# Kernel tuning notes

Measured on AMD Instinct MI355X. Metric: run time of the kernel, lower is better.

## Reference

```python
import jax, jax.numpy as jnp
import numpy as np

N_NODES = 100_000
N_EDGES = 1_200_000
IN_C, HID_C, OUT_C, K = 64, 64, 32, 3


def setup_inputs() -> dict:
    key = jax.random.key(0)
    ks = jax.random.split(key, 8)
    x = jax.random.normal(ks[0], (N_NODES, IN_C), dtype=jnp.float32)
    edge_index = jax.random.randint(ks[1], (2, N_EDGES), 0, N_NODES, dtype=jnp.int64)
    # ChebConv parameters: weight [K, in, out], bias [out] (Glorot-ish scale)
    W1 = jax.random.normal(ks[2], (K, IN_C, HID_C), dtype=jnp.float32) / np.sqrt(IN_C)
    b1 = jnp.zeros((HID_C,), dtype=jnp.float32)
    W2 = jax.random.normal(ks[3], (K, HID_C, OUT_C), dtype=jnp.float32) / np.sqrt(HID_C)
    b2 = jnp.zeros((OUT_C,), dtype=jnp.float32)
    return {"x": x, "edge_index": edge_index, "W1": W1, "b1": b1, "W2": W2, "b2": b2}


def _cheb_conv(x, row, col, norm_w, W, b):
    # Scaled Laplacian with lambda_max=2 (PyG default): L_hat = -D^{-1/2} A D^{-1/2}
    def prop(t):  # L_hat @ t, via edge gather + segment-sum scatter
        msg = norm_w[:, None] * t[col]            # [E, C]
        return -jax.ops.segment_sum(msg, row, num_segments=N_NODES)

    Tx0 = x
    out = Tx0 @ W[0]
    Tx1 = prop(x)
    out = out + Tx1 @ W[1]
    for k in range(2, W.shape[0]):
        Tx2 = 2.0 * prop(Tx1) - Tx0          # Chebyshev recurrence
        out = out + Tx2 @ W[k]
        Tx0, Tx1 = Tx1, Tx2
    return out + b


def reference(x, edge_index, W1, b1, W2, b2):
    row, col = edge_index[0], edge_index[1]
    deg = jax.ops.segment_sum(jnp.ones((row.shape[0],), x.dtype), row,
                              num_segments=N_NODES)
    deg_inv_sqrt = jnp.where(deg > 0, jax.lax.rsqrt(jnp.maximum(deg, 1.0)), 0.0)
    norm_w = deg_inv_sqrt[row] * deg_inv_sqrt[col]   # symmetric normalization

    h = jax.nn.relu(_cheb_conv(x, row, col, norm_w, W1, b1))
    # dropout omitted (eval mode / training=False)
    return _cheb_conv(h, row, col, norm_w, W2, b2)
```

## Files before the change

kernel.cpp:

```cpp
#include <hip/hip_runtime.h>
#include <hip/hip_fp16.h>

#define N_NODES_C 100000
#define N_EDGES_C 1200000
#define NBUK ((N_NODES_C + 255) >> 8)
#define CHUNK 4096

typedef _Float16 f16x8 __attribute__((ext_vector_type(8)));
typedef float f32x4 __attribute__((ext_vector_type(4)));

#define PACK(r8, c) ((c) | ((r8) << 17))
#define UNPACK_C(v) ((v) & 0x1FFFF)
#define UNPACK_R(v) ((v) >> 17)

__global__ __launch_bounds__(256) void hist_f2h(const int* __restrict__ ei,
                                                int* __restrict__ bucket_cnt,
                                                const float* __restrict__ x,
                                                __half* __restrict__ xh,
                                                int nedges, int n4, int histB) {
    __shared__ int cnt[NBUK];
    const int tid = threadIdx.x;
    if (blockIdx.x < histB) {
        const int base = blockIdx.x * CHUNK;
        const int nloc = min(CHUNK, nedges - base);
        for (int i = tid; i < NBUK; i += 256) cnt[i] = 0;
        __syncthreads();
        for (int i = tid; i < nloc; i += 256) atomicAdd(&cnt[ei[base + i] >> 8], 1);
        __syncthreads();
        for (int b = tid; b < NBUK; b += 256) {
            int n = cnt[b];
            if (n) atomicAdd(&bucket_cnt[b], n);
        }
    } else {
        int i = (blockIdx.x - histB) * 256 + tid;
        if (i < n4) {
            float4 v = ((const float4*)x)[i];
            __half2 tmp[2];
            tmp[0] = __floats2half2_rn(v.x, v.y);
            tmp[1] = __floats2half2_rn(v.z, v.w);
            ((float2*)xh)[i] = *(float2*)tmp;
        }
    }
}

__global__ __launch_bounds__(256) void scan_fold(const int* __restrict__ bucket_cnt,
                                                 int* __restrict__ bucket_base,
                                                 int* __restrict__ bucket_next, int nb,
                                                 const float* __restrict__ W1,
                                                 const float* __restrict__ W2,
                                                 __half* __restrict__ W1f,
                                                 __half* __restrict__ W2f) {
    const int tid = threadIdx.x;
    if (blockIdx.x == 0) {
        __shared__ int s[256];
        int a0 = (2 * tid < nb) ? bucket_cnt[2 * tid] : 0;
        int a1 = (2 * tid + 1 < nb) ? bucket_cnt[2 * tid + 1] : 0;
        s[tid] = a0 + a1;
        __syncthreads();
        for (int off = 1; off < 256; off <<= 1) {
            int v = s[tid];
            int add = (tid >= off) ? s[tid - off] : 0;
            __syncthreads();
            s[tid] = v + add;
            __syncthreads();
        }
        int excl = (tid > 0) ? s[tid - 1] : 0;
        if (2 * tid < nb) { bucket_base[2 * tid] = excl; bucket_next[2 * tid] = excl; }
        if (2 * tid + 1 < nb) { bucket_base[2 * tid + 1] = excl + a0; bucket_next[2 * tid + 1] = excl + a0; }
        if (tid == 255) bucket_base[nb] = s[255];
        return;
    }
    int i = (blockIdx.x - 1) * 256 + tid;
    if (i < 12288) {
        int j = i & 7;
        int lane = (i >> 3) & 63;
        int rest = i >> 9;
        int kh = rest % 6;
        int ct = rest / 6;
        int term = kh >> 1;
        int k = ((kh & 1) << 5) | ((lane >> 4) << 3) | j;
        int c = (ct << 4) | (lane & 15);
        float w0 = W1[k * 64 + c];
        float w1 = W1[4096 + k * 64 + c];
        float w2 = W1[2 * 4096 + k * 64 + c];
        float v = (term == 0) ? (w0 - w2) : ((term == 1) ? w1 : 2.0f * w2);
        W1f[i] = __float2half(v);
    } else if (i < 12288 + 6144) {
        int ii = i - 12288;
        int j = ii & 7;
        int lane = (ii >> 3) & 63;
        int rest = ii >> 9;
        int kh = rest & 1;
        int ct = rest >> 1;
        int k = (kh << 5) | ((lane >> 4) << 3) | j;
        int cg = ct * 16 + (lane & 15);
        int seg = cg >> 5;
        int c = cg & 31;
        float w0 = W2[k * 32 + c];
        float w1 = W2[2048 + k * 32 + c];
        float w2 = W2[2 * 2048 + k * 32 + c];
        float v = (seg == 0) ? (w0 - w2) : ((seg == 1) ? w1 : 2.0f * w2);
        W2f[ii] = __float2half(v);
    }
}

__global__ __launch_bounds__(256) void bin_stage(const int* __restrict__ ei,
                                                 int* __restrict__ bucket_next,
                                                 int* __restrict__ staged, int nedges) {
    __shared__ int cnt[NBUK];
    __shared__ int ofs[NBUK];
    __shared__ int run[NBUK];
    __shared__ int gbase[NBUK];
    __shared__ int ssum[256];
    __shared__ int2 sedge[CHUNK];
    const int tid = threadIdx.x;
    const int base = blockIdx.x * CHUNK;
    const int nloc = min(CHUNK, nedges - base);

    for (int i = tid; i < NBUK; i += 256) { cnt[i] = 0; run[i] = 0; }
    __syncthreads();

    int r[16], c[16];
#pragma unroll
    for (int k = 0; k < 16; ++k) {
        int loc = tid + k * 256;
        bool ok = loc < nloc;
        int idx = base + loc;
        r[k] = ok ? ei[idx] : -1;
        c[k] = ok ? ei[nedges + idx] : 0;
        if (ok) atomicAdd(&cnt[r[k] >> 8], 1);
    }
    __syncthreads();

    int a0 = (2 * tid < NBUK) ? cnt[2 * tid] : 0;
    int a1 = (2 * tid + 1 < NBUK) ? cnt[2 * tid + 1] : 0;
    ssum[tid] = a0 + a1;
    __syncthreads();
    for (int off = 1; off < 256; off <<= 1) {
        int v = ssum[tid];
        int add = (tid >= off) ? ssum[tid - off] : 0;
        __syncthreads();
        ssum[tid] = v + add;
        __syncthreads();
    }
    int excl = (tid > 0) ? ssum[tid - 1] : 0;
    if (2 * tid < NBUK) ofs[2 * tid] = excl;
    if (2 * tid + 1 < NBUK) ofs[2 * tid + 1] = excl + a0;
    __syncthreads();

#pragma unroll
    for (int k = 0; k < 16; ++k) {
        if (r[k] >= 0) {
            int b = r[k] >> 8;
            int p = atomicAdd(&run[b], 1);
            sedge[ofs[b] + p] = make_int2(r[k], c[k]);
        }
    }
    __syncthreads();

    for (int b = tid; b < NBUK; b += 256) {
        int n = cnt[b];
        gbase[b] = n ? atomicAdd(&bucket_next[b], n) : 0;
    }
    __syncthreads();

    for (int i = tid; i < nloc; i += 256) {
        int2 e = sedge[i];
        int b = e.x >> 8;
        staged[gbase[b] + (i - ofs[b])] = PACK(e.x & 255, e.y);
    }
}

__global__ __launch_bounds__(256) void bin_count(const int* __restrict__ staged,
                                                 const int* __restrict__ bucket_base,
                                                 int* __restrict__ rowptr, float* __restrict__ dis,
                                                 int nnodes, int nedges) {
    __shared__ int deg[256];
    __shared__ int ssum[256];
    const int b = blockIdx.x;
    const int n0 = b << 8;
    const int nend = min(n0 + 256, nnodes);
    const int nloc = nend - n0;
    const int tid = threadIdx.x;
    deg[tid] = 0;
    __syncthreads();
    const int ebase = bucket_base[b];
    const int ecount = bucket_base[b + 1] - ebase;
    for (int i = tid; i < ecount; i += 256) {
        atomicAdd(&deg[UNPACK_R(staged[ebase + i])], 1);
    }
    __syncthreads();
    int d = deg[tid];
    if (tid < nloc) {
        float df = (float)d;
        dis[n0 + tid] = (d > 0) ? (1.0f / sqrtf(fmaxf(df, 1.f))) : 0.f;
    }
    ssum[tid] = d;
    __syncthreads();
    for (int off = 1; off < 256; off <<= 1) {
        int v = ssum[tid];
        int add = (tid >= off) ? ssum[tid - off] : 0;
        __syncthreads();
        ssum[tid] = v + add;
        __syncthreads();
    }
    int excl = (tid > 0) ? ssum[tid - 1] : 0;
    if (tid < nloc) rowptr[n0 + tid] = ebase + excl;
    if (b == NBUK - 1 && tid == 0) rowptr[nnodes] = nedges;
}

__global__ __launch_bounds__(256) void bin_place(const int* __restrict__ staged,
                                                 const int* __restrict__ rowptr,
                                                 const float* __restrict__ dis,
                                                 int2* __restrict__ colw, int nnodes) {
    __shared__ int rp[256];
    __shared__ int nx[256];
    __shared__ float dl[256];
    const int b = blockIdx.x;
    const int n0 = b << 8;
    const int nend = min(n0 + 256, nnodes);
    const int nloc = nend - n0;
    const int tid = threadIdx.x;
    if (tid < nloc) {
        rp[tid] = rowptr[n0 + tid];
        dl[tid] = dis[n0 + tid];
    }
    nx[tid] = 0;
    __syncthreads();
    const int ebase = rowptr[n0];
    const int ecount = rowptr[nend] - ebase;
    for (int i = tid; i < ecount; i += 256) {
        int v = staged[ebase + i];
        int col = UNPACK_C(v);
        int rrel = UNPACK_R(v);
        int p = atomicAdd(&nx[rrel], 1);
        float w = -dl[rrel] * dis[col];
        colw[rp[rrel] + p] = make_int2(col, __float_as_int(w));
    }
}

__global__ __launch_bounds__(256) void prop_gather_h(const __half* __restrict__ t,
                                                     const int* __restrict__ rowptr,
                                                     const int2* __restrict__ colw,
                                                     __half* __restrict__ out, int nnodes) {
    int grp = threadIdx.x >> 3;
    int ln = threadIdx.x & 7;
    int node = blockIdx.x * 32 + grp;
    if (node >= nnodes) return;
    int s = rowptr[node];
    int e = rowptr[node + 1];
    float acc[8] = {0.f, 0.f, 0.f, 0.f, 0.f, 0.f, 0.f, 0.f};
    int i = s;
    for (; i + 3 < e; i += 4) {
        int2 cw0 = colw[i];
        int2 cw1 = colw[i + 1];
        int2 cw2 = colw[i + 2];
        int2 cw3 = colw[i + 3];
        float4 r0 = ((const float4*)(t + (size_t)cw0.x * 64))[ln];
        float4 r1 = ((const float4*)(t + (size_t)cw1.x * 64))[ln];
        float4 r2 = ((const float4*)(t + (size_t)cw2.x * 64))[ln];
        float4 r3 = ((const float4*)(t + (size_t)cw3.x * 64))[ln];
        float w0 = __int_as_float(cw0.y);
        float w1 = __int_as_float(cw1.y);
        float w2 = __int_as_float(cw2.y);
        float w3 = __int_as_float(cw3.y);
        const __half2* h0 = (const __half2*)&r0;
        const __half2* h1 = (const __half2*)&r1;
        const __half2* h2 = (const __half2*)&r2;
        const __half2* h3 = (const __half2*)&r3;
#pragma unroll
        for (int q = 0; q < 4; ++q) {
            float2 f0 = __half22float2(h0[q]);
            float2 f1 = __half22float2(h1[q]);
            float2 f2 = __half22float2(h2[q]);
            float2 f3 = __half22float2(h3[q]);
            acc[2 * q + 0] += w0 * f0.x + w1 * f1.x + w2 * f2.x + w3 * f3.x;
            acc[2 * q + 1] += w0 * f0.y + w1 * f1.y + w2 * f2.y + w3 * f3.y;
        }
    }
    for (; i < e; ++i) {
        int2 cw0 = colw[i];
        float w0 = __int_as_float(cw0.y);
        float4 r0 = ((const float4*)(t + (size_t)cw0.x * 64))[ln];
        const __half2* h0 = (const __half2*)&r0;
#pragma unroll
        for (int q = 0; q < 4; ++q) {
            float2 f0 = __half22float2(h0[q]);
            acc[2 * q + 0] += w0 * f0.x;
            acc[2 * q + 1] += w0 * f0.y;
        }
    }
    __half2 tmp[4];
    tmp[0] = __floats2half2_rn(acc[0], acc[1]);
    tmp[1] = __floats2half2_rn(acc[2], acc[3]);
    tmp[2] = __floats2half2_rn(acc[4], acc[5]);
    tmp[3] = __floats2half2_rn(acc[6], acc[7]);
    ((float4*)(out + (size_t)node * 64))[ln] = *(float4*)tmp;
}

template <bool F32OUT>
__global__ __launch_bounds__(256) void prop_gather32(const __half* __restrict__ t,
                                                     const int* __restrict__ rowptr,
                                                     const int2* __restrict__ colw,
                                                     const void* __restrict__ addin,
                                                     void* __restrict__ outv, int nnodes) {
    int grp = threadIdx.x >> 2;
    int ln = threadIdx.x & 3;
    int node = blockIdx.x * 64 + grp;
    if (node >= nnodes) return;
    int s = rowptr[node];
    int e = rowptr[node + 1];
    float acc[8] = {0.f, 0.f, 0.f, 0.f, 0.f, 0.f, 0.f, 0.f};
    int i = s;
    for (; i + 3 < e; i += 4) {
        int2 cw0 = colw[i];
        int2 cw1 = colw[i + 1];
        int2 cw2 = colw[i + 2];
        int2 cw3 = colw[i + 3];
        float4 r0 = ((const float4*)(t + (size_t)cw0.x * 32))[ln];
        float4 r1 = ((const float4*)(t + (size_t)cw1.x * 32))[ln];
        float4 r2 = ((const float4*)(t + (size_t)cw2.x * 32))[ln];
        float4 r3 = ((const float4*)(t + (size_t)cw3.x * 32))[ln];
        float w0 = __int_as_float(cw0.y);
        float w1 = __int_as_float(cw1.y);
        float w2 = __int_as_float(cw2.y);
        float w3 = __int_as_float(cw3.y);
        const __half2* h0 = (const __half2*)&r0;
        const __half2* h1 = (const __half2*)&r1;
        const __half2* h2 = (const __half2*)&r2;
        const __half2* h3 = (const __half2*)&r3;
#pragma unroll
        for (int q = 0; q < 4; ++q) {
            float2 f0 = __half22float2(h0[q]);
            float2 f1 = __half22float2(h1[q]);
            float2 f2 = __half22float2(h2[q]);
            float2 f3 = __half22float2(h3[q]);
            acc[2 * q + 0] += w0 * f0.x + w1 * f1.x + w2 * f2.x + w3 * f3.x;
            acc[2 * q + 1] += w0 * f0.y + w1 * f1.y + w2 * f2.y + w3 * f3.y;
        }
    }
    for (; i < e; ++i) {
        int2 cw0 = colw[i];
        float w0 = __int_as_float(cw0.y);
        float4 r0 = ((const float4*)(t + (size_t)cw0.x * 32))[ln];
        const __half2* h0 = (const __half2*)&r0;
#pragma unroll
        for (int q = 0; q < 4; ++q) {
            float2 f0 = __half22float2(h0[q]);
            acc[2 * q + 0] += w0 * f0.x;
            acc[2 * q + 1] += w0 * f0.y;
        }
    }
    if (F32OUT) {
        const float* add = (const float*)addin;
        float* out = (float*)outv;
        float4 a0 = ((const float4*)(add + (size_t)node * 32))[ln * 2 + 0];
        float4 a1 = ((const float4*)(add + (size_t)node * 32))[ln * 2 + 1];
        a0.x += acc[0]; a0.y += acc[1]; a0.z += acc[2]; a0.w += acc[3];
        a1.x += acc[4]; a1.y += acc[5]; a1.z += acc[6]; a1.w += acc[7];
        ((float4*)(out + (size_t)node * 32))[ln * 2 + 0] = a0;
        ((float4*)(out + (size_t)node * 32))[ln * 2 + 1] = a1;
    } else {
        const __half* add = (const __half*)addin;
        __half* out = (__half*)outv;
        float4 raw = ((const float4*)(add + (size_t)node * 32))[ln];
        const __half2* hp = (const __half2*)&raw;
        float2 a0 = __half22float2(hp[0]);
        float2 a1 = __half22float2(hp[1]);
        float2 a2 = __half22float2(hp[2]);
        float2 a3 = __half22float2(hp[3]);
        __half2 tmp[4];
        tmp[0] = __floats2half2_rn(acc[0] + a0.x, acc[1] + a0.y);
        tmp[1] = __floats2half2_rn(acc[2] + a1.x, acc[3] + a1.y);
        tmp[2] = __floats2half2_rn(acc[4] + a2.x, acc[5] + a2.y);
        tmp[3] = __floats2half2_rn(acc[6] + a3.x, acc[7] + a3.y);
        ((float4*)(out + (size_t)node * 32))[ln] = *(float4*)tmp;
    }
}

__global__ __launch_bounds__(256) void gemm_fused(const __half* __restrict__ A0,
                                                  const __half* __restrict__ A1,
                                                  const __half* __restrict__ A2,
                                                  const __half* __restrict__ W1f,
                                                  const float* __restrict__ b1,
                                                  const __half* __restrict__ W2f,
                                                  const float* __restrict__ b2,
                                                  float* __restrict__ P0,
                                                  __half* __restrict__ G1,
                                                  __half* __restrict__ G2, int nnodes) {
    __shared__ __align__(16) __half htile[4][16 * 72];
    const int wave = threadIdx.x >> 6;
    const int lane = threadIdx.x & 63;
    const int node0 = blockIdx.x * 64 + wave * 16;
    const int m = lane & 15;
    const int quad = lane >> 4;
    int arow = node0 + m;
    if (arow >= nnodes) arow = nnodes - 1;

    const __half* Ap[3] = {A0, A1, A2};
    f16x8 a[6];
#pragma unroll
    for (int kh = 0; kh < 6; ++kh) {
        const __half* A = Ap[kh >> 1];
        a[kh] = *(const f16x8*)(A + (size_t)arow * 64 + ((kh & 1) << 5) + (quad << 3));
    }
    __half* ht = htile[wave];
#pragma unroll
    for (int ct = 0; ct < 4; ++ct) {
        f32x4 acc = {0.f, 0.f, 0.f, 0.f};
#pragma unroll
        for (int kh = 0; kh < 6; ++kh) {
            f16x8 b = *(const f16x8*)(W1f + ((size_t)(ct * 6 + kh) * 64 + lane) * 8);
            acc = __builtin_amdgcn_mfma_f32_16x16x32_f16(a[kh], b, acc, 0, 0, 0);
        }
        int col = (ct << 4) | m;
        float bias = b1[col];
#pragma unroll
        for (int r = 0; r < 4; ++r) {
            ht[(quad * 4 + r) * 72 + col] = __float2half(fmaxf(acc[r] + bias, 0.f));
        }
    }
    __syncthreads();

    f16x8 h0 = *(const f16x8*)(ht + m * 72 + (quad << 3));
    f16x8 h1 = *(const f16x8*)(ht + m * 72 + 32 + (quad << 3));
#pragma unroll
    for (int ct = 0; ct < 6; ++ct) {
        f32x4 acc = {0.f, 0.f, 0.f, 0.f};
        f16x8 b0 = *(const f16x8*)(W2f + ((size_t)(ct * 2 + 0) * 64 + lane) * 8);
        f16x8 b1v = *(const f16x8*)(W2f + ((size_t)(ct * 2 + 1) * 64 + lane) * 8);
        acc = __builtin_amdgcn_mfma_f32_16x16x32_f16(h0, b0, acc, 0, 0, 0);
        acc = __builtin_amdgcn_mfma_f32_16x16x32_f16(h1, b1v, acc, 0, 0, 0);
        int seg = ct >> 1;
        int c = ((ct & 1) << 4) | m;
#pragma unroll
        for (int r = 0; r < 4; ++r) {
            int n = node0 + (quad << 2) + r;
            if (n >= nnodes) continue;
            float v = acc[r];
            if (seg == 0)      P0[(size_t)n * 32 + c] = v + b2[c];
            else if (seg == 1) G1[(size_t)n * 32 + c] = __float2half(v);
            else               G2[(size_t)n * 32 + c] = __float2half(v);
        }
    }
}

extern "C" void kernel_launch(void* const* d_in, const int* in_sizes, int n_in,
                              void* d_out, int out_size, void* d_ws, size_t ws_size,
                              hipStream_t stream) {
    const float* x  = (const float*)d_in[0];
    const int*   ei = (const int*)d_in[1];
    const float* W1 = (const float*)d_in[2];
    const float* b1 = (const float*)d_in[3];
    const float* W2 = (const float*)d_in[4];
    const float* b2 = (const float*)d_in[5];
    float* out = (float*)d_out;

    const int NN = N_NODES_C;
    const int NE = N_EDGES_C;
    const size_t HFEAT_BYTES = (size_t)NN * 64 * sizeof(__half);
    const size_t H32_BYTES = (size_t)NN * 32 * sizeof(__half);

    char* ws = (char*)d_ws;
    size_t off = 0;
    auto alloc = [&](size_t bytes) -> void* {
        void* p = ws + off;
        off += (bytes + 255) & ~(size_t)255;
        return p;
    };
    int*    bucket_cnt  = (int*)alloc((size_t)NBUK * 4);
    int*    bucket_base = (int*)alloc((size_t)(NBUK + 1) * 4);
    int*    bucket_next = (int*)alloc((size_t)NBUK * 4);
    int*    rowptr      = (int*)alloc((size_t)(NN + 1) * 4);
    float*  dis         = (float*)alloc((size_t)NN * 4);
    int*    staged      = (int*)alloc((size_t)NE * 4);
    int2*   colw        = (int2*)alloc((size_t)NE * 8);
    __half* xh          = (__half*)alloc(HFEAT_BYTES);
    __half* T1h         = (__half*)alloc(HFEAT_BYTES);
    __half* T2h         = (__half*)alloc(HFEAT_BYTES);
    __half* Qh          = (__half*)alloc(H32_BYTES);
    float*  P0          = (float*)alloc((size_t)NN * 32 * 4);
    __half* W1f         = (__half*)alloc((size_t)4 * 6 * 64 * 8 * 2);
    __half* W2f         = (__half*)alloc((size_t)6 * 2 * 64 * 8 * 2);

    const int PROPB = (NN + 31) / 32;
    const int PROP32B = (NN + 63) / 64;
    const int CONV4 = NN * 64 / 4;
    const int CONVB = (CONV4 + 255) / 256;
    const int BINB = (NE + CHUNK - 1) / CHUNK;
    const int GEMMB = (NN + 63) / 64;
    const int FOLDB = 1 + (18432 + 255) / 256;

    hipMemsetAsync(bucket_cnt, 0, (size_t)NBUK * 4, stream);
    hist_f2h<<<BINB + CONVB, 256, 0, stream>>>(ei, bucket_cnt, x, xh, NE, CONV4, BINB);
    scan_fold<<<FOLDB, 256, 0, stream>>>(bucket_cnt, bucket_base, bucket_next, NBUK,
                                         W1, W2, W1f, W2f);
    bin_stage<<<BINB, 256, 0, stream>>>(ei, bucket_next, staged, NE);
    bin_count<<<NBUK, 256, 0, stream>>>(staged, bucket_base, rowptr, dis, NN, NE);
    bin_place<<<NBUK, 256, 0, stream>>>(staged, rowptr, dis, colw, NN);

    prop_gather_h<<<PROPB, 256, 0, stream>>>(xh, rowptr, colw, T1h, NN);
    prop_gather_h<<<PROPB, 256, 0, stream>>>(T1h, rowptr, colw, T2h, NN);
    gemm_fused<<<GEMMB, 256, 0, stream>>>(xh, T1h, T2h, W1f, b1, W2f, b2, P0, T1h, T2h, NN);

    prop_gather32<false><<<PROP32B, 256, 0, stream>>>(T2h, rowptr, colw, T1h, Qh, NN);
    prop_gather32<true><<<PROP32B, 256, 0, stream>>>(Qh, rowptr, colw, P0, out, NN);
}
```

Before: 244.8 us.

## Store CSR as column-only, merge count and place, degree-sort node order

The count and place binning kernels are merged into one. It keeps staged edges in LDS so they are read once, and it writes a column-only CSR instead of (col, weight) pairs. The propagation kernels now compute edge weights on the fly from a per-node dis array, which halves the index stream they read but adds a gather on dis. A new kernel buckets nodes by degree into a permutation so that groups in a block have similar edge counts, reducing divergence. The bin chunk size also drops, and nontemporal loads and stores are added for the streamed data.

New measurement: 316.8 us. +29.4%, slower.

```diff
diff --git a/kernel.cpp b/kernel.cpp
--- a/kernel.cpp
+++ b/kernel.cpp
@@ -4,7 +4,9 @@
 #define N_NODES_C 100000
 #define N_EDGES_C 1200000
 #define NBUK ((N_NODES_C + 255) >> 8)
-#define CHUNK 4096
+#define CHUNK 2048
+#define DCAP 4096
+#define DBINS 64
 
 typedef _Float16 f16x8 __attribute__((ext_vector_type(8)));
 typedef float f32x4 __attribute__((ext_vector_type(4)));
@@ -120,9 +122,9 @@
     for (int i = tid; i < NBUK; i += 256) { cnt[i] = 0; run[i] = 0; }
     __syncthreads();
 
-    int r[16], c[16];
-#pragma unroll
-    for (int k = 0; k < 16; ++k) {
+    int r[8], c[8];
+#pragma unroll
+    for (int k = 0; k < 8; ++k) {
         int loc = tid + k * 256;
         bool ok = loc < nloc;
         int idx = base + loc;
@@ -149,7 +151,7 @@
     __syncthreads();
 
 #pragma unroll
-    for (int k = 0; k < 16; ++k) {
+    for (int k = 0; k < 8; ++k) {
         if (r[k] >= 0) {
             int b = r[k] >> 8;
             int p = atomicAdd(&run[b], 1);
@@ -167,33 +169,45 @@
     for (int i = tid; i < nloc; i += 256) {
         int2 e = sedge[i];
         int b = e.x >> 8;
-        staged[gbase[b] + (i - ofs[b])] = PACK(e.x & 255, e.y);
-    }
-}
-
-__global__ __launch_bounds__(256) void bin_count(const int* __restrict__ staged,
-                                                 const int* __restrict__ bucket_base,
-                                                 int* __restrict__ rowptr, float* __restrict__ dis,
-                                                 int nnodes, int nedges) {
+        __builtin_nontemporal_store(PACK(e.x & 255, e.y), staged + gbase[b] + (i - ofs[b]));
+    }
+}
+
+__global__ __launch_bounds__(256) void bin_count_place(const int* __restrict__ staged,
+                                                       const int* __restrict__ bucket_base,
+                                                       int* __restrict__ rowptr,
+                                                       float* __restrict__ dis,
+                                                       int* __restrict__ colz,
+                                                       int* __restrict__ deghist,
+                                                       int nnodes, int nedges) {
     __shared__ int deg[256];
     __shared__ int ssum[256];
+    __shared__ int rp[256];
+    __shared__ int nx[256];
+    __shared__ int dh[DBINS];
+    __shared__ int cache[DCAP];
     const int b = blockIdx.x;
     const int n0 = b << 8;
     const int nend = min(n0 + 256, nnodes);
     const int nloc = nend - n0;
     const int tid = threadIdx.x;
     deg[tid] = 0;
+    nx[tid] = 0;
+    if (tid < DBINS) dh[tid] = 0;
     __syncthreads();
     const int ebase = bucket_base[b];
     const int ecount = bucket_base[b + 1] - ebase;
     for (int i = tid; i < ecount; i += 256) {
-        atomicAdd(&deg[UNPACK_R(staged[ebase + i])], 1);
+        int v = __builtin_nontemporal_load(staged + ebase + i);
+        if (i < DCAP) cache[i] = v;
+        atomicAdd(&deg[UNPACK_R(v)], 1);
     }
     __syncthreads();
     int d = deg[tid];
     if (tid < nloc) {
         float df = (float)d;
         dis[n0 + tid] = (d > 0) ? (1.0f / sqrtf(fmaxf(df, 1.f))) : 0.f;
+        atomicAdd(&dh[min(d, DBINS - 1)], 1);
     }
     ssum[tid] = d;
     __syncthreads();
@@ -205,65 +219,83 @@
         __syncthreads();
     }
     int excl = (tid > 0) ? ssum[tid - 1] : 0;
+    rp[tid] = ebase + excl;
     if (tid < nloc) rowptr[n0 + tid] = ebase + excl;
     if (b == NBUK - 1 && tid == 0) rowptr[nnodes] = nedges;
-}
-
-__global__ __launch_bounds__(256) void bin_place(const int* __restrict__ staged,
-                                                 const int* __restrict__ rowptr,
-                                                 const float* __restrict__ dis,
-                                                 int2* __restrict__ colw, int nnodes) {
-    __shared__ int rp[256];
-    __shared__ int nx[256];
-    __shared__ float dl[256];
-    const int b = blockIdx.x;
-    const int n0 = b << 8;
-    const int nend = min(n0 + 256, nnodes);
-    const int nloc = nend - n0;
+    if (tid < DBINS) {
+        int cn = dh[tid];
+        if (cn) atomicAdd(&deghist[tid], cn);
+    }
+    __syncthreads();
+    for (int i = tid; i < ecount; i += 256) {
+        int v = (i < DCAP) ? cache[i] : staged[ebase + i];
+        int rrel = UNPACK_R(v);
+        int col = UNPACK_C(v);
+        int p = atomicAdd(&nx[rrel], 1);
+        __builtin_nontemporal_store(col, colz + rp[rrel] + p);
+    }
+}
+
+__global__ __launch_bounds__(256) void deg_scatter(const int* __restrict__ rowptr,
+                                                   const int* __restrict__ deghist,
+                                                   int* __restrict__ dnext,
+                                                   int* __restrict__ perm, int nnodes) {
+    __shared__ int gbase[DBINS];
+    __shared__ int lcnt[DBINS];
+    __shared__ int lbase[DBINS];
     const int tid = threadIdx.x;
-    if (tid < nloc) {
-        rp[tid] = rowptr[n0 + tid];
-        dl[tid] = dis[n0 + tid];
-    }
-    nx[tid] = 0;
-    __syncthreads();
-    const int ebase = rowptr[n0];
-    const int ecount = rowptr[nend] - ebase;
-    for (int i = tid; i < ecount; i += 256) {
-        int v = staged[ebase + i];
-        int col = UNPACK_C(v);
-        int rrel = UNPACK_R(v);
-        int p = atomicAdd(&nx[rrel], 1);
-        float w = -dl[rrel] * dis[col];
-        colw[rp[rrel] + p] = make_int2(col, __float_as_int(w));
-    }
+    if (tid == 0) {
+        int runv = 0;
+        for (int i = 0; i < DBINS; ++i) { gbase[i] = runv; runv += deghist[i]; }
+    }
+    if (tid < DBINS) lcnt[tid] = 0;
+    __syncthreads();
+    int n = blockIdx.x * 256 + tid;
+    int bn = 0, lp = 0;
+    bool ok = n < nnodes;
+    if (ok) {
+        int d = rowptr[n + 1] - rowptr[n];
+        bn = min(d, DBINS - 1);
+        lp = atomicAdd(&lcnt[bn], 1);
+    }
+    __syncthreads();
+    if (tid < DBINS) {
+        int cn = lcnt[tid];
+        lbase[tid] = cn ? atomicAdd(&dnext[tid], cn) : 0;
+    }
+    __syncthreads();
+    if (ok) perm[gbase[bn] + lbase[bn] + lp] = n;
 }
 
 __global__ __launch_bounds__(256) void prop_gather_h(const __half* __restrict__ t,
                                                      const int* __restrict__ rowptr,
-                                                     const int2* __restrict__ colw,
+                                                     const int* __restrict__ colz,
+                                                     const float* __restrict__ dis,
+                                                     const int* __restrict__ perm,
                                                      __half* __restrict__ out, int nnodes) {
     int grp = threadIdx.x >> 3;
     int ln = threadIdx.x & 7;
-    int node = blockIdx.x * 32 + grp;
-    if (node >= nnodes) return;
+    int idx = blockIdx.x * 32 + grp;
+    if (idx >= nnodes) return;
+    int node = perm[idx];
     int s = rowptr[node];
     int e = rowptr[node + 1];
+    float nds = -dis[node];
     float acc[8] = {0.f, 0.f, 0.f, 0.f, 0.f, 0.f, 0.f, 0.f};
     int i = s;
     for (; i + 3 < e; i += 4) {
-        int2 cw0 = colw[i];
-        int2 cw1 = colw[i + 1];
-        int2 cw2 = colw[i + 2];
-        int2 cw3 = colw[i + 3];
-        float4 r0 = ((const float4*)(t + (size_t)cw0.x * 64))[ln];
-        float4 r1 = ((const float4*)(t + (size_t)cw1.x * 64))[ln];
-        float4 r2 = ((const float4*)(t + (size_t)cw2.x * 64))[ln];
-        float4 r3 = ((const float4*)(t + (size_t)cw3.x * 64))[ln];
-        float w0 = __int_as_float(cw0.y);
-        float w1 = __int_as_float(cw1.y);
-        float w2 = __int_as_float(cw2.y);
-        float w3 = __int_as_float(cw3.y);
+        int c0 = __builtin_nontemporal_load(colz + i);
+        int c1 = __builtin_nontemporal_load(colz + i + 1);
+        int c2 = __builtin_nontemporal_load(colz + i + 2);
+        int c3 = __builtin_nontemporal_load(colz + i + 3);
+        float4 r0 = ((const float4*)(t + (size_t)c0 * 64))[ln];
+        float4 r1 = ((const float4*)(t + (size_t)c1 * 64))[ln];
+        float4 r2 = ((const float4*)(t + (size_t)c2 * 64))[ln];
+        float4 r3 = ((const float4*)(t + (size_t)c3 * 64))[ln];
+        float w0 = nds * dis[c0];
+        float w1 = nds * dis[c1];
+        float w2 = nds * dis[c2];
+        float w3 = nds * dis[c3];
         const __half2* h0 = (const __half2*)&r0;
         const __half2* h1 = (const __half2*)&r1;
         const __half2* h2 = (const __half2*)&r2;
@@ -279,9 +311,9 @@
         }
     }
     for (; i < e; ++i) {
-        int2 cw0 = colw[i];
-        float w0 = __int_as_float(cw0.y);
-        float4 r0 = ((const float4*)(t + (size_t)cw0.x * 64))[ln];
+        int c0 = __builtin_nontemporal_load(colz + i);
+        float w0 = nds * dis[c0];
+        float4 r0 = ((const float4*)(t + (size_t)c0 * 64))[ln];
         const __half2* h0 = (const __half2*)&r0;
 #pragma unroll
         for (int q = 0; q < 4; ++q) {
@@ -301,30 +333,34 @@
 template <bool F32OUT>
 __global__ __launch_bounds__(256) void prop_gather32(const __half* __restrict__ t,
                                                      const int* __restrict__ rowptr,
-                                                     const int2* __restrict__ colw,
+                                                     const int* __restrict__ colz,
+                                                     const float* __restrict__ dis,
+                                                     const int* __restrict__ perm,
                                                      const void* __restrict__ addin,
                                                      void* __restrict__ outv, int nnodes) {
     int grp = threadIdx.x >> 2;
     int ln = threadIdx.x & 3;
-    int node = blockIdx.x * 64 + grp;
-    if (node >= nnodes) return;
+    int idx = blockIdx.x * 64 + grp;
+    if (idx >= nnodes) return;
+    int node = perm[idx];
     int s = rowptr[node];
     int e = rowptr[node + 1];
+    float nds = -dis[node];
     float acc[8] = {0.f, 0.f, 0.f, 0.f, 0.f, 0.f, 0.f, 0.f};
     int i = s;
     for (; i + 3 < e; i += 4) {
-        int2 cw0 = colw[i];
-        int2 cw1 = colw[i + 1];
-        int2 cw2 = colw[i + 2];
-        int2 cw3 = colw[i + 3];
-        float4 r0 = ((const float4*)(t + (size_t)cw0.x * 32))[ln];
-        float4 r1 = ((const float4*)(t + (size_t)cw1.x * 32))[ln];
-        float4 r2 = ((const float4*)(t + (size_t)cw2.x * 32))[ln];
-        float4 r3 = ((const float4*)(t + (size_t)cw3.x * 32))[ln];
-        float w0 = __int_as_float(cw0.y);
-        float w1 = __int_as_float(cw1.y);
-        float w2 = __int_as_float(cw2.y);
-        float w3 = __int_as_float(cw3.y);
+        int c0 = __builtin_nontemporal_load(colz + i);
+        int c1 = __builtin_nontemporal_load(colz + i + 1);
+        int c2 = __builtin_nontemporal_load(colz + i + 2);
+        int c3 = __builtin_nontemporal_load(colz + i + 3);
+        float4 r0 = ((const float4*)(t + (size_t)c0 * 32))[ln];
+        float4 r1 = ((const float4*)(t + (size_t)c1 * 32))[ln];
+        float4 r2 = ((const float4*)(t + (size_t)c2 * 32))[ln];
+        float4 r3 = ((const float4*)(t + (size_t)c3 * 32))[ln];
+        float w0 = nds * dis[c0];
+        float w1 = nds * dis[c1];
+        float w2 = nds * dis[c2];
+        float w3 = nds * dis[c3];
         const __half2* h0 = (const __half2*)&r0;
         const __half2* h1 = (const __half2*)&r1;
         const __half2* h2 = (const __half2*)&r2;
@@ -340,9 +376,9 @@
         }
     }
     for (; i < e; ++i) {
-        int2 cw0 = colw[i];
-        float w0 = __int_as_float(cw0.y);
-        float4 r0 = ((const float4*)(t + (size_t)cw0.x * 32))[ln];
+        int c0 = __builtin_nontemporal_load(colz + i);
+        float w0 = nds * dis[c0];
+        float4 r0 = ((const float4*)(t + (size_t)c0 * 32))[ln];
         const __half2* h0 = (const __half2*)&r0;
 #pragma unroll
         for (int q = 0; q < 4; ++q) {
@@ -469,12 +505,15 @@
         return p;
     };
     int*    bucket_cnt  = (int*)alloc((size_t)NBUK * 4);
+    int*    deghist     = (int*)alloc((size_t)DBINS * 4);
+    int*    dnext       = (int*)alloc((size_t)DBINS * 4);
     int*    bucket_base = (int*)alloc((size_t)(NBUK + 1) * 4);
     int*    bucket_next = (int*)alloc((size_t)NBUK * 4);
     int*    rowptr      = (int*)alloc((size_t)(NN + 1) * 4);
     float*  dis         = (float*)alloc((size_t)NN * 4);
+    int*    perm        = (int*)alloc((size_t)NN * 4);
     int*    staged      = (int*)alloc((size_t)NE * 4);
-    int2*   colw        = (int2*)alloc((size_t)NE * 8);
+    int*    colz        = (int*)alloc((size_t)NE * 4);
     __half* xh          = (__half*)alloc(HFEAT_BYTES);
     __half* T1h         = (__half*)alloc(HFEAT_BYTES);
     __half* T2h         = (__half*)alloc(HFEAT_BYTES);
@@ -490,19 +529,22 @@
     const int BINB = (NE + CHUNK - 1) / CHUNK;
     const int GEMMB = (NN + 63) / 64;
     const int FOLDB = 1 + (18432 + 255) / 256;
-
-    hipMemsetAsync(bucket_cnt, 0, (size_t)NBUK * 4, stream);
+    const int SCATB = (NN + 255) / 256;
+
+    size_t zbytes = (size_t)((char*)dnext - (char*)bucket_cnt) + 256;
+    hipMemsetAsync(bucket_cnt, 0, zbytes, stream);
     hist_f2h<<<BINB + CONVB, 256, 0, stream>>>(ei, bucket_cnt, x, xh, NE, CONV4, BINB);
     scan_fold<<<FOLDB, 256, 0, stream>>>(bucket_cnt, bucket_base, bucket_next, NBUK,
                                          W1, W2, W1f, W2f);
     bin_stage<<<BINB, 256, 0, stream>>>(ei, bucket_next, staged, NE);
-    bin_count<<<NBUK, 256, 0, stream>>>(staged, bucket_base, rowptr, dis, NN, NE);
-    bin_place<<<NBUK, 256, 0, stream>>>(staged, rowptr, dis, colw, NN);
-
-    prop_gather_h<<<PROPB, 256, 0, stream>>>(xh, rowptr, colw, T1h, NN);
-    prop_gather_h<<<PROPB, 256, 0, stream>>>(T1h, rowptr, colw, T2h, NN);
+    bin_count_place<<<NBUK, 256, 0, stream>>>(staged, bucket_base, rowptr, dis, colz,
+                                              deghist, NN, NE);
+    deg_scatter<<<SCATB, 256, 0, stream>>>(rowptr, deghist, dnext, perm, NN);
+
+    prop_gather_h<<<PROPB, 256, 0, stream>>>(xh, rowptr, colz, dis, perm, T1h, NN);
+    prop_gather_h<<<PROPB, 256, 0, stream>>>(T1h, rowptr, colz, dis, perm, T2h, NN);
     gemm_fused<<<GEMMB, 256, 0, stream>>>(xh, T1h, T2h, W1f, b1, W2f, b2, P0, T1h, T2h, NN);
 
-    prop_gather32<false><<<PROP32B, 256, 0, stream>>>(T2h, rowptr, colw, T1h, Qh, NN);
-    prop_gather32<true><<<PROP32B, 256, 0, stream>>>(Qh, rowptr, colw, P0, out, NN);
-}
+    prop_gather32<false><<<PROP32B, 256, 0, stream>>>(T2h, rowptr, colz, dis, perm, T1h, Qh, NN);
+    prop_gather32<true><<<PROP32B, 256, 0, stream>>>(Qh, rowptr, colz, dis, perm, P0, out, NN);
+}
```

## Sort nodes by degree so gather wavefronts process similar-degree rows

Applied to the files above, without the earlier changes.

Builds a degree histogram in bin_count and a counting-sort permutation of nodes by degree (capped at 64 bins) in extra blocks of bin_place. All four gather kernels then process nodes in permuted order, so lanes within a wavefront handle rows of similar length and divergence and tail imbalance are reduced. The cost is an extra permutation array, an indirection per node, and less locality in output writes and rowptr reads. The memset is widened to also zero the new histogram counters.

After: 256.8 us. +4.9%, slower.

```diff
diff --git a/kernel.cpp b/kernel.cpp
--- a/kernel.cpp
+++ b/kernel.cpp
@@ -5,6 +5,7 @@
 #define N_EDGES_C 1200000
 #define NBUK ((N_NODES_C + 255) >> 8)
 #define CHUNK 4096
+#define DBINS 64
 
 typedef _Float16 f16x8 __attribute__((ext_vector_type(8)));
 typedef float f32x4 __attribute__((ext_vector_type(4)));
@@ -174,15 +175,18 @@
 __global__ __launch_bounds__(256) void bin_count(const int* __restrict__ staged,
                                                  const int* __restrict__ bucket_base,
                                                  int* __restrict__ rowptr, float* __restrict__ dis,
+                                                 int* __restrict__ deghist,
                                                  int nnodes, int nedges) {
     __shared__ int deg[256];
     __shared__ int ssum[256];
+    __shared__ int dh[DBINS];
     const int b = blockIdx.x;
     const int n0 = b << 8;
     const int nend = min(n0 + 256, nnodes);
     const int nloc = nend - n0;
     const int tid = threadIdx.x;
     deg[tid] = 0;
+    if (tid < DBINS) dh[tid] = 0;
     __syncthreads();
     const int ebase = bucket_base[b];
     const int ecount = bucket_base[b + 1] - ebase;
@@ -194,6 +198,7 @@
     if (tid < nloc) {
         float df = (float)d;
         dis[n0 + tid] = (d > 0) ? (1.0f / sqrtf(fmaxf(df, 1.f))) : 0.f;
+        atomicAdd(&dh[min(d, DBINS - 1)], 1);
     }
     ssum[tid] = d;
     __syncthreads();
@@ -207,12 +212,47 @@
     int excl = (tid > 0) ? ssum[tid - 1] : 0;
     if (tid < nloc) rowptr[n0 + tid] = ebase + excl;
     if (b == NBUK - 1 && tid == 0) rowptr[nnodes] = nedges;
+    if (tid < DBINS) {
+        int cn = dh[tid];
+        if (cn) atomicAdd(&deghist[tid], cn);
+    }
 }
 
 __global__ __launch_bounds__(256) void bin_place(const int* __restrict__ staged,
                                                  const int* __restrict__ rowptr,
                                                  const float* __restrict__ dis,
-                                                 int2* __restrict__ colw, int nnodes) {
+                                                 int2* __restrict__ colw,
+                                                 const int* __restrict__ deghist,
+                                                 int* __restrict__ dnext,
+                                                 int* __restrict__ perm, int nnodes) {
+    const int tid = threadIdx.x;
+    if (blockIdx.x >= NBUK) {
+        __shared__ int gbase[DBINS];
+        __shared__ int lcnt[DBINS];
+        __shared__ int lbase[DBINS];
+        if (tid == 0) {
+            int runv = 0;
+            for (int i = 0; i < DBINS; ++i) { gbase[i] = runv; runv += deghist[i]; }
+        }
+        if (tid < DBINS) lcnt[tid] = 0;
+        __syncthreads();
+        int n = (blockIdx.x - NBUK) * 256 + tid;
+        int bn = 0, lp = 0;
+        bool ok = n < nnodes;
+        if (ok) {
+            int d = rowptr[n + 1] - rowptr[n];
+            bn = min(d, DBINS - 1);
+            lp = atomicAdd(&lcnt[bn], 1);
+        }
+        __syncthreads();
+        if (tid < DBINS) {
+            int cn = lcnt[tid];
+            lbase[tid] = cn ? atomicAdd(&dnext[tid], cn) : 0;
+        }
+        __syncthreads();
+        if (ok) perm[gbase[bn] + lbase[bn] + lp] = n;
+        return;
+    }
     __shared__ int rp[256];
     __shared__ int nx[256];
     __shared__ float dl[256];
@@ -220,7 +260,6 @@
     const int n0 = b << 8;
     const int nend = min(n0 + 256, nnodes);
     const int nloc = nend - n0;
-    const int tid = threadIdx.x;
     if (tid < nloc) {
         rp[tid] = rowptr[n0 + tid];
         dl[tid] = dis[n0 + tid];
@@ -242,11 +281,13 @@
 __global__ __launch_bounds__(256) void prop_gather_h(const __half* __restrict__ t,
                                                      const int* __restrict__ rowptr,
                                                      const int2* __restrict__ colw,
+                                                     const int* __restrict__ perm,
                                                      __half* __restrict__ out, int nnodes) {
     int grp = threadIdx.x >> 3;
     int ln = threadIdx.x & 7;
-    int node = blockIdx.x * 32 + grp;
-    if (node >= nnodes) return;
+    int idx = blockIdx.x * 32 + grp;
+    if (idx >= nnodes) return;
+    int node = perm[idx];
     int s = rowptr[node];
     int e = rowptr[node + 1];
     float acc[8] = {0.f, 0.f, 0.f, 0.f, 0.f, 0.f, 0.f, 0.f};
@@ -302,12 +343,14 @@
 __global__ __launch_bounds__(256) void prop_gather32(const __half* __restrict__ t,
                                                      const int* __restrict__ rowptr,
                                                      const int2* __restrict__ colw,
+                                                     const int* __restrict__ perm,
                                                      const void* __restrict__ addin,
                                                      void* __restrict__ outv, int nnodes) {
     int grp = threadIdx.x >> 2;
     int ln = threadIdx.x & 3;
-    int node = blockIdx.x * 64 + grp;
-    if (node >= nnodes) return;
+    int idx = blockIdx.x * 64 + grp;
+    if (idx >= nnodes) return;
+    int node = perm[idx];
     int s = rowptr[node];
     int e = rowptr[node + 1];
     float acc[8] = {0.f, 0.f, 0.f, 0.f, 0.f, 0.f, 0.f, 0.f};
@@ -469,10 +512,13 @@
         return p;
     };
     int*    bucket_cnt  = (int*)alloc((size_t)NBUK * 4);
+    int*    deghist     = (int*)alloc((size_t)DBINS * 4);
+    int*    dnext       = (int*)alloc((size_t)DBINS * 4);
     int*    bucket_base = (int*)alloc((size_t)(NBUK + 1) * 4);
     int*    bucket_next = (int*)alloc((size_t)NBUK * 4);
     int*    rowptr      = (int*)alloc((size_t)(NN + 1) * 4);
     float*  dis         = (float*)alloc((size_t)NN * 4);
+    int*    perm        = (int*)alloc((size_t)NN * 4);
     int*    staged      = (int*)alloc((size_t)NE * 4);
     int2*   colw        = (int2*)alloc((size_t)NE * 8);
     __half* xh          = (__half*)alloc(HFEAT_BYTES);
@@ -490,19 +536,22 @@
     const int BINB = (NE + CHUNK - 1) / CHUNK;
     const int GEMMB = (NN + 63) / 64;
     const int FOLDB = 1 + (18432 + 255) / 256;
-
-    hipMemsetAsync(bucket_cnt, 0, (size_t)NBUK * 4, stream);
+    const int SCATB = (NN + 255) / 256;
+
+    size_t zbytes = (size_t)((char*)bucket_base - (char*)bucket_cnt);
+    hipMemsetAsync(bucket_cnt, 0, zbytes, stream);
     hist_f2h<<<BINB + CONVB, 256, 0, stream>>>(ei, bucket_cnt, x, xh, NE, CONV4, BINB);
     scan_fold<<<FOLDB, 256, 0, stream>>>(bucket_cnt, bucket_base, bucket_next, NBUK,
                                          W1, W2, W1f, W2f);
     bin_stage<<<BINB, 256, 0, stream>>>(ei, bucket_next, staged, NE);
-    bin_count<<<NBUK, 256, 0, stream>>>(staged, bucket_base, rowptr, dis, NN, NE);
-    bin_place<<<NBUK, 256, 0, stream>>>(staged, rowptr, dis, colw, NN);
-
-    prop_gather_h<<<PROPB, 256, 0, stream>>>(xh, rowptr, colw, T1h, NN);
-    prop_gather_h<<<PROPB, 256, 0, stream>>>(T1h, rowptr, colw, T2h, NN);
+    bin_count<<<NBUK, 256, 0, stream>>>(staged, bucket_base, rowptr, dis, deghist, NN, NE);
+    bin_place<<<NBUK + SCATB, 256, 0, stream>>>(staged, rowptr, dis, colw,
+                                                deghist, dnext, perm, NN);
+
+    prop_gather_h<<<PROPB, 256, 0, stream>>>(xh, rowptr, colw, perm, T1h, NN);
+    prop_gather_h<<<PROPB, 256, 0, stream>>>(T1h, rowptr, colw, perm, T2h, NN);
     gemm_fused<<<GEMMB, 256, 0, stream>>>(xh, T1h, T2h, W1f, b1, W2f, b2, P0, T1h, T2h, NN);
 
-    prop_gather32<false><<<PROP32B, 256, 0, stream>>>(T2h, rowptr, colw, T1h, Qh, NN);
-    prop_gather32<true><<<PROP32B, 256, 0, stream>>>(Qh, rowptr, colw, P0, out, NN);
-}
+    prop_gather32<false><<<PROP32B, 256, 0, stream>>>(T2h, rowptr, colw, perm, T1h, Qh, NN);
+    prop_gather32<true><<<PROP32B, 256, 0, stream>>>(Qh, rowptr, colw, perm, P0, out, NN);
+}
```

## Replace bucketed two-pass CSR build with global degree atomics and direct placement

Applied to the files above, without the earlier changes.

Replaces the bucket-staging CSR construction (bin_stage, bin_count, bin_place) with per-node global degree atomics in the histogram kernel, a per-bucket rowptr/dis scan, and a direct placement kernel that uses global atomics on a per-node cursor. This removes the staged intermediate array and one kernel launch, and drops the shared-memory sorting passes. In exchange it relies on many scattered global atomics on 100K counters, which may contend or be slower than the LDS-local work. Edge order within a row becomes nondeterministic, which can perturb floating-point summation order.

New measurement: 319.3 us. 30.4% more time.

```diff
diff --git a/kernel.cpp b/kernel.cpp
--- a/kernel.cpp
+++ b/kernel.cpp
@@ -9,15 +9,12 @@
 typedef _Float16 f16x8 __attribute__((ext_vector_type(8)));
 typedef float f32x4 __attribute__((ext_vector_type(4)));
 
-#define PACK(r8, c) ((c) | ((r8) << 17))
-#define UNPACK_C(v) ((v) & 0x1FFFF)
-#define UNPACK_R(v) ((v) >> 17)
-
-__global__ __launch_bounds__(256) void hist_f2h(const int* __restrict__ ei,
-                                                int* __restrict__ bucket_cnt,
-                                                const float* __restrict__ x,
-                                                __half* __restrict__ xh,
-                                                int nedges, int n4, int histB) {
+__global__ __launch_bounds__(256) void hist_deg_f2h(const int* __restrict__ ei,
+                                                    int* __restrict__ bucket_cnt,
+                                                    int* __restrict__ deg,
+                                                    const float* __restrict__ x,
+                                                    __half* __restrict__ xh,
+                                                    int nedges, int n4, int histB) {
     __shared__ int cnt[NBUK];
     const int tid = threadIdx.x;
     if (blockIdx.x < histB) {
@@ -25,7 +22,11 @@
         const int nloc = min(CHUNK, nedges - base);
         for (int i = tid; i < NBUK; i += 256) cnt[i] = 0;
         __syncthreads();
-        for (int i = tid; i < nloc; i += 256) atomicAdd(&cnt[ei[base + i] >> 8], 1);
+        for (int i = tid; i < nloc; i += 256) {
+            int r = ei[base + i];
+            atomicAdd(&cnt[r >> 8], 1);
+            atomicAdd(&deg[r], 1);
+        }
         __syncthreads();
         for (int b = tid; b < NBUK; b += 256) {
             int n = cnt[b];
@@ -44,8 +45,7 @@
 }
 
 __global__ __launch_bounds__(256) void scan_fold(const int* __restrict__ bucket_cnt,
-                                                 int* __restrict__ bucket_base,
-                                                 int* __restrict__ bucket_next, int nb,
+                                                 int* __restrict__ bucket_base, int nb,
                                                  const float* __restrict__ W1,
                                                  const float* __restrict__ W2,
                                                  __half* __restrict__ W1f,
@@ -65,8 +65,8 @@
             __syncthreads();
         }
         int excl = (tid > 0) ? s[tid - 1] : 0;
-        if (2 * tid < nb) { bucket_base[2 * tid] = excl; bucket_next[2 * tid] = excl; }
-        if (2 * tid + 1 < nb) { bucket_base[2 * tid + 1] = excl + a0; bucket_next[2 * tid + 1] = excl + a0; }
+        if (2 * tid < nb) bucket_base[2 * tid] = excl;
+        if (2 * tid + 1 < nb) bucket_base[2 * tid + 1] = excl + a0;
         if (tid == 255) bucket_base[nb] = s[255];
         return;
     }
@@ -104,93 +104,19 @@
     }
 }
 
-__global__ __launch_bounds__(256) void bin_stage(const int* __restrict__ ei,
-                                                 int* __restrict__ bucket_next,
-                                                 int* __restrict__ staged, int nedges) {
-    __shared__ int cnt[NBUK];
-    __shared__ int ofs[NBUK];
-    __shared__ int run[NBUK];
-    __shared__ int gbase[NBUK];
-    __shared__ int ssum[256];
-    __shared__ int2 sedge[CHUNK];
-    const int tid = threadIdx.x;
-    const int base = blockIdx.x * CHUNK;
-    const int nloc = min(CHUNK, nedges - base);
-
-    for (int i = tid; i < NBUK; i += 256) { cnt[i] = 0; run[i] = 0; }
-    __syncthreads();
-
-    int r[16], c[16];
-#pragma unroll
-    for (int k = 0; k < 16; ++k) {
-        int loc = tid + k * 256;
-        bool ok = loc < nloc;
-        int idx = base + loc;
-        r[k] = ok ? ei[idx] : -1;
-        c[k] = ok ? ei[nedges + idx] : 0;
-        if (ok) atomicAdd(&cnt[r[k] >> 8], 1);
-    }
-    __syncthreads();
-
-    int a0 = (2 * tid < NBUK) ? cnt[2 * tid] : 0;
-    int a1 = (2 * tid + 1 < NBUK) ? cnt[2 * tid + 1] : 0;
-    ssum[tid] = a0 + a1;
-    __syncthreads();
-    for (int off = 1; off < 256; off <<= 1) {
-        int v = ssum[tid];
-        int add = (tid >= off) ? ssum[tid - off] : 0;
-        __syncthreads();
-        ssum[tid] = v + add;
-        __syncthreads();
-    }
-    int excl = (tid > 0) ? ssum[tid - 1] : 0;
-    if (2 * tid < NBUK) ofs[2 * tid] = excl;
-    if (2 * tid + 1 < NBUK) ofs[2 * tid + 1] = excl + a0;
-    __syncthreads();
-
-#pragma unroll
-    for (int k = 0; k < 16; ++k) {
-        if (r[k] >= 0) {
-            int b = r[k] >> 8;
-            int p = atomicAdd(&run[b], 1);
-            sedge[ofs[b] + p] = make_int2(r[k], c[k]);
-        }
-    }
-    __syncthreads();
-
-    for (int b = tid; b < NBUK; b += 256) {
-        int n = cnt[b];
-        gbase[b] = n ? atomicAdd(&bucket_next[b], n) : 0;
-    }
-    __syncthreads();
-
-    for (int i = tid; i < nloc; i += 256) {
-        int2 e = sedge[i];
-        int b = e.x >> 8;
-        staged[gbase[b] + (i - ofs[b])] = PACK(e.x & 255, e.y);
-    }
-}
-
-__global__ __launch_bounds__(256) void bin_count(const int* __restrict__ staged,
-                                                 const int* __restrict__ bucket_base,
-                                                 int* __restrict__ rowptr, float* __restrict__ dis,
-                                                 int nnodes, int nedges) {
-    __shared__ int deg[256];
+__global__ __launch_bounds__(256) void rowptr_dis(const int* __restrict__ deg,
+                                                  const int* __restrict__ bucket_base,
+                                                  int* __restrict__ rowptr,
+                                                  int* __restrict__ nextc,
+                                                  float* __restrict__ dis,
+                                                  int nnodes, int nedges) {
     __shared__ int ssum[256];
     const int b = blockIdx.x;
     const int n0 = b << 8;
     const int nend = min(n0 + 256, nnodes);
     const int nloc = nend - n0;
     const int tid = threadIdx.x;
-    deg[tid] = 0;
-    __syncthreads();
-    const int ebase = bucket_base[b];
-    const int ecount = bucket_base[b + 1] - ebase;
-    for (int i = tid; i < ecount; i += 256) {
-        atomicAdd(&deg[UNPACK_R(staged[ebase + i])], 1);
-    }
-    __syncthreads();
-    int d = deg[tid];
+    int d = (tid < nloc) ? deg[n0 + tid] : 0;
     if (tid < nloc) {
         float df = (float)d;
         dis[n0 + tid] = (d > 0) ? (1.0f / sqrtf(fmaxf(df, 1.f))) : 0.f;
@@ -205,37 +131,30 @@
         __syncthreads();
     }
     int excl = (tid > 0) ? ssum[tid - 1] : 0;
-    if (tid < nloc) rowptr[n0 + tid] = ebase + excl;
+    if (tid < nloc) {
+        int rp = bucket_base[b] + excl;
+        rowptr[n0 + tid] = rp;
+        nextc[n0 + tid] = rp;
+    }
     if (b == NBUK - 1 && tid == 0) rowptr[nnodes] = nedges;
 }
 
-__global__ __launch_bounds__(256) void bin_place(const int* __restrict__ staged,
-                                                 const int* __restrict__ rowptr,
-                                                 const float* __restrict__ dis,
-                                                 int2* __restrict__ colw, int nnodes) {
-    __shared__ int rp[256];
-    __shared__ int nx[256];
-    __shared__ float dl[256];
-    const int b = blockIdx.x;
-    const int n0 = b << 8;
-    const int nend = min(n0 + 256, nnodes);
-    const int nloc = nend - n0;
+__global__ __launch_bounds__(256) void place(const int* __restrict__ ei,
+                                             const float* __restrict__ dis,
+                                             int* __restrict__ nextc,
+                                             int2* __restrict__ colw, int nedges) {
+    const int base = blockIdx.x * 1024;
     const int tid = threadIdx.x;
-    if (tid < nloc) {
-        rp[tid] = rowptr[n0 + tid];
-        dl[tid] = dis[n0 + tid];
-    }
-    nx[tid] = 0;
-    __syncthreads();
-    const int ebase = rowptr[n0];
-    const int ecount = rowptr[nend] - ebase;
-    for (int i = tid; i < ecount; i += 256) {
-        int v = staged[ebase + i];
-        int col = UNPACK_C(v);
-        int rrel = UNPACK_R(v);
-        int p = atomicAdd(&nx[rrel], 1);
-        float w = -dl[rrel] * dis[col];
-        colw[rp[rrel] + p] = make_int2(col, __float_as_int(w));
+#pragma unroll
+    for (int k = 0; k < 4; ++k) {
+        int idx = base + k * 256 + tid;
+        if (idx < nedges) {
+            int r = ei[idx];
+            int c = ei[nedges + idx];
+            float w = -dis[r] * dis[c];
+            int p = atomicAdd(&nextc[r], 1);
+            colw[p] = make_int2(c, __float_as_int(w));
+        }
     }
 }
 
@@ -469,11 +388,11 @@
         return p;
     };
     int*    bucket_cnt  = (int*)alloc((size_t)NBUK * 4);
+    int*    deg         = (int*)alloc((size_t)NN * 4);
     int*    bucket_base = (int*)alloc((size_t)(NBUK + 1) * 4);
-    int*    bucket_next = (int*)alloc((size_t)NBUK * 4);
     int*    rowptr      = (int*)alloc((size_t)(NN + 1) * 4);
+    int*    nextc       = (int*)alloc((size_t)NN * 4);
     float*  dis         = (float*)alloc((size_t)NN * 4);
-    int*    staged      = (int*)alloc((size_t)NE * 4);
     int2*   colw        = (int2*)alloc((size_t)NE * 8);
     __half* xh          = (__half*)alloc(HFEAT_BYTES);
     __half* T1h         = (__half*)alloc(HFEAT_BYTES);
@@ -490,14 +409,16 @@
     const int BINB = (NE + CHUNK - 1) / CHUNK;
     const int GEMMB = (NN + 63) / 64;
     const int FOLDB = 1 + (18432 + 255) / 256;
-
-    hipMemsetAsync(bucket_cnt, 0, (size_t)NBUK * 4, stream);
-    hist_f2h<<<BINB + CONVB, 256, 0, stream>>>(ei, bucket_cnt, x, xh, NE, CONV4, BINB);
-    scan_fold<<<FOLDB, 256, 0, stream>>>(bucket_cnt, bucket_base, bucket_next, NBUK,
+    const int PLACEB = (NE + 1023) / 1024;
+
+    size_t zbytes = (size_t)((char*)bucket_base - (char*)bucket_cnt);
+    hipMemsetAsync(bucket_cnt, 0, zbytes, stream);
+    hist_deg_f2h<<<BINB + CONVB, 256, 0, stream>>>(ei, bucket_cnt, deg, x, xh,
+                                                   NE, CONV4, BINB);
+    scan_fold<<<FOLDB, 256, 0, stream>>>(bucket_cnt, bucket_base, NBUK,
                                          W1, W2, W1f, W2f);
-    bin_stage<<<BINB, 256, 0, stream>>>(ei, bucket_next, staged, NE);
-    bin_count<<<NBUK, 256, 0, stream>>>(staged, bucket_base, rowptr, dis, NN, NE);
-    bin_place<<<NBUK, 256, 0, stream>>>(staged, rowptr, dis, colw, NN);
+    rowptr_dis<<<NBUK, 256, 0, stream>>>(deg, bucket_base, rowptr, nextc, dis, NN, NE);
+    place<<<PLACEB, 256, 0, stream>>>(ei, dis, nextc, colw, NE);
 
     prop_gather_h<<<PROPB, 256, 0, stream>>>(xh, rowptr, colw, T1h, NN);
     prop_gather_h<<<PROPB, 256, 0, stream>>>(T1h, rowptr, colw, T2h, NN);
```
